# Kernel tuning notes

Measured on AMD Instinct MI355X. Metric: run time of the kernel, lower is better.

## Reference

```python
import jax, jax.numpy as jnp
import numpy as np

N = 100000        # nodes
E = 3200000       # edges (avg degree 32)
IN, HID, OUT = 512, 256, 64
K = 10
ALPHA = 0.1


def setup_inputs() -> dict:
    key = jax.random.key(0)
    k1, k2, k3, k4 = jax.random.split(key, 4)
    x = jax.random.normal(k1, (N, IN), dtype=jnp.float32)
    edge_index = jax.random.randint(k2, (2, E), 0, N, dtype=jnp.int64)
    W1 = jax.random.normal(k3, (IN, HID), dtype=jnp.float32) * (1.0 / np.sqrt(IN))
    b1 = jnp.zeros((HID,), dtype=jnp.float32)
    W2 = jax.random.normal(k4, (HID, OUT), dtype=jnp.float32) * (1.0 / np.sqrt(HID))
    b2 = jnp.zeros((OUT,), dtype=jnp.float32)
    return {"x": x, "edge_index": edge_index, "W1": W1, "b1": b1, "W2": W2, "b2": b2}


def reference(x, edge_index, W1, b1, W2, b2):
    # MLP head: Linear -> ReLU -> Linear
    h = jax.nn.relu(x @ W1 + b1)
    h = h @ W2 + b2                                   # [N, OUT]

    # gcn_norm with self-loops: D^-1/2 (A + I) D^-1/2
    src = jnp.concatenate([edge_index[0], jnp.arange(N, dtype=edge_index.dtype)])
    dst = jnp.concatenate([edge_index[1], jnp.arange(N, dtype=edge_index.dtype)])
    deg = jax.ops.segment_sum(jnp.ones_like(src, dtype=h.dtype), dst, num_segments=N)
    dinv = jnp.where(deg > 0, jax.lax.rsqrt(deg), 0.0)
    norm = dinv[src] * dinv[dst]                      # [E+N]

    h0 = h

    def step(h, _):
        msg = h[src] * norm[:, None]                  # gather + edge scale
        agg = jax.ops.segment_sum(msg, dst, num_segments=N)  # scatter-add
        h = (1.0 - ALPHA) * agg + ALPHA * h0          # teleport
        return h, None

    h, _ = jax.lax.scan(step, h, None, length=K)
    return h
```

## Files before the change

### kernel.cpp

```cpp
#include <hip/hip_runtime.h>
#include <hip/hip_bf16.h>
#include <hip/hip_fp16.h>


typedef __bf16 bf16x8 __attribute__((ext_vector_type(8)));
typedef float f32x4 __attribute__((ext_vector_type(4)));

static constexpr int IN = 512, HID = 256, OUT = 64;
static constexpr int LDT = 40;

static __device__ __forceinline__ ushort f2bf(float f) {
  __hip_bfloat16 b = __float2bfloat16(f);
  return *reinterpret_cast<ushort*>(&b);
}
static __device__ __forceinline__ float bf2f(ushort u) {
  unsigned int x = ((unsigned int)u) << 16;
  return __uint_as_float(x);
}
static __device__ __forceinline__ float h15f(unsigned int u) {
  ushort hb = (ushort)(u & 0x7FFFu);
  __half h = *reinterpret_cast<__half*>(&hb);
  return __half2float(h);
}

__global__ void transpose_f32_bf16(const float* __restrict__ in, ushort* __restrict__ out,
                                   int K, int C) {
  int idx = blockIdx.x * 256 + threadIdx.x;
  if (idx < K * C) {
    int n = idx / K, k = idx % K;
    out[idx] = f2bf(in[k * C + n]);
  }
}

__global__ __launch_bounds__(256) void gemm1(const float* __restrict__ X,
                                             const ushort* __restrict__ W1T,
                                             const float* __restrict__ b1,
                                             ushort* __restrict__ h1, int M) {
  __shared__ __align__(16) ushort As[128 * LDT];
  __shared__ __align__(16) ushort Bs[128 * LDT];
  const int tid = threadIdx.x;
  const int m0 = blockIdx.x * 128;
  const int n0 = blockIdx.y * 128;
  const int lane = tid & 63, w = tid >> 6;
  const int wr = w >> 1, wc = w & 1;
  const int lm = lane & 15, lq = lane >> 4;
  const int cB = tid & 3, rB = tid >> 2;
  const int cA = tid & 7, rA = tid >> 3;

  f32x4 acc[4][4] = {};

  for (int k0 = 0; k0 < IN; k0 += 32) {
#pragma unroll
    for (int rr = 0; rr < 4; ++rr) {
      int m = rA + rr * 32;
      int gm = m0 + m; gm = gm < M ? gm : M - 1;
      float4 f = *reinterpret_cast<const float4*>(&X[(size_t)gm * IN + k0 + cA * 4]);
      ushort4 cv;
      cv.x = f2bf(f.x); cv.y = f2bf(f.y); cv.z = f2bf(f.z); cv.w = f2bf(f.w);
      *reinterpret_cast<ushort4*>(&As[m * LDT + cA * 4]) = cv;
    }
#pragma unroll
    for (int rr = 0; rr < 2; ++rr) {
      int n = rB + rr * 64;
      *reinterpret_cast<int4*>(&Bs[n * LDT + cB * 8]) =
          *reinterpret_cast<const int4*>(&W1T[(size_t)(n0 + n) * IN + k0 + cB * 8]);
    }
    __syncthreads();
    bf16x8 af[4], bq[4];
#pragma unroll
    for (int mi = 0; mi < 4; ++mi)
      af[mi] = *reinterpret_cast<const bf16x8*>(&As[(wr * 64 + mi * 16 + lm) * LDT + lq * 8]);
#pragma unroll
    for (int ni = 0; ni < 4; ++ni)
      bq[ni] = *reinterpret_cast<const bf16x8*>(&Bs[(wc * 64 + ni * 16 + lm) * LDT + lq * 8]);
#pragma unroll
    for (int mi = 0; mi < 4; ++mi)
#pragma unroll
      for (int ni = 0; ni < 4; ++ni)
        acc[mi][ni] = __builtin_amdgcn_mfma_f32_16x16x32_bf16(af[mi], bq[ni], acc[mi][ni], 0, 0, 0);
    __syncthreads();
  }

#pragma unroll
  for (int ni = 0; ni < 4; ++ni) {
    int col = n0 + wc * 64 + ni * 16 + lm;
    float bias = b1[col];
#pragma unroll
    for (int mi = 0; mi < 4; ++mi) {
#pragma unroll
      for (int rg = 0; rg < 4; ++rg) {
        int row = m0 + wr * 64 + mi * 16 + lq * 4 + rg;
        if (row < M) {
          float v = acc[mi][ni][rg] + bias;
          v = v > 0.f ? v : 0.f;
          h1[(size_t)row * HID + col] = f2bf(v);
        }
      }
    }
  }
}

__global__ __launch_bounds__(256) void gemm2(const ushort* __restrict__ h1,
                                             const ushort* __restrict__ W2T,
                                             const float* __restrict__ b2,
                                             float* __restrict__ H0f,
                                             ushort* __restrict__ H0b, int M) {
  __shared__ __align__(16) ushort As[128 * LDT];
  __shared__ __align__(16) ushort Bs[64 * LDT];
  const int tid = threadIdx.x;
  const int m0 = blockIdx.x * 128;
  const int lane = tid & 63, w = tid >> 6;
  const int lm = lane & 15, lq = lane >> 4;
  const int c = tid & 3, r = tid >> 2;

  f32x4 acc[2][4] = {};

  for (int k0 = 0; k0 < HID; k0 += 32) {
#pragma unroll
    for (int rr = 0; rr < 2; ++rr) {
      int m = r + rr * 64;
      int gm = m0 + m; gm = gm < M ? gm : M - 1;
      *reinterpret_cast<int4*>(&As[m * LDT + c * 8]) =
          *reinterpret_cast<const int4*>(&h1[(size_t)gm * HID + k0 + c * 8]);
    }
    *reinterpret_cast<int4*>(&Bs[r * LDT + c * 8]) =
        *reinterpret_cast<const int4*>(&W2T[(size_t)r * HID + k0 + c * 8]);
    __syncthreads();
    bf16x8 af[2], bq[4];
#pragma unroll
    for (int mi = 0; mi < 2; ++mi)
      af[mi] = *reinterpret_cast<const bf16x8*>(&As[(w * 32 + mi * 16 + lm) * LDT + lq * 8]);
#pragma unroll
    for (int ni = 0; ni < 4; ++ni)
      bq[ni] = *reinterpret_cast<const bf16x8*>(&Bs[(ni * 16 + lm) * LDT + lq * 8]);
#pragma unroll
    for (int mi = 0; mi < 2; ++mi)
#pragma unroll
      for (int ni = 0; ni < 4; ++ni)
        acc[mi][ni] = __builtin_amdgcn_mfma_f32_16x16x32_bf16(af[mi], bq[ni], acc[mi][ni], 0, 0, 0);
    __syncthreads();
  }

#pragma unroll
  for (int ni = 0; ni < 4; ++ni) {
    int col = ni * 16 + lm;
    float bias = b2[col];
#pragma unroll
    for (int mi = 0; mi < 2; ++mi) {
#pragma unroll
      for (int rg = 0; rg < 4; ++rg) {
        int row = m0 + w * 32 + mi * 16 + lq * 4 + rg;
        if (row < M) {
          float v = acc[mi][ni][rg] + bias;
          H0f[(size_t)row * OUT + col] = v;
          H0b[(size_t)row * OUT + col] = f2bf(v);
        }
      }
    }
  }
}

__global__ void count_deg(const int* __restrict__ ei, int* __restrict__ cnt, int E) {
  int e = blockIdx.x * 256 + threadIdx.x;
  if (e < E) atomicAdd(&cnt[ei[E + e]], 1);
}

__global__ void calc_dinv(const int* __restrict__ cnt, float* __restrict__ dinv, int n) {
  int v = blockIdx.x * 256 + threadIdx.x;
  if (v < n) dinv[v] = rsqrtf((float)cnt[v] + 1.0f);
}

__global__ __launch_bounds__(1024) void scan_kernel(const int* __restrict__ cnt,
                                                    int* __restrict__ offs,
                                                    int* __restrict__ cursor, int n) {
  __shared__ int wsum[16];
  __shared__ int woff[16];
  __shared__ int carry_s;
  const int tid = threadIdx.x;
  const int lane = tid & 63, wid = tid >> 6;
  if (tid == 0) carry_s = 0;
  __syncthreads();
  for (int base = 0; base < n; base += 4096) {
    int i0 = base + tid * 4;
    int x[4];
#pragma unroll
    for (int j = 0; j < 4; ++j) x[j] = (i0 + j < n) ? cnt[i0 + j] : 0;
    int tsum = x[0] + x[1] + x[2] + x[3];
    int val = tsum;
#pragma unroll
    for (int d = 1; d < 64; d <<= 1) {
      int t = __shfl_up(val, d, 64);
      if (lane >= d) val += t;
    }
    if (lane == 63) wsum[wid] = val;
    __syncthreads();
    if (wid == 0) {
      int s = (lane < 16) ? wsum[lane] : 0;
      int sv = s;
#pragma unroll
      for (int d = 1; d < 16; d <<= 1) {
        int t = __shfl_up(sv, d, 64);
        if (lane >= d) sv += t;
      }
      if (lane < 16) woff[lane] = sv - s;
    }
    __syncthreads();
    int excl = carry_s + woff[wid] + (val - tsum);
#pragma unroll
    for (int j = 0; j < 4; ++j) {
      if (i0 + j < n) { offs[i0 + j] = excl; cursor[i0 + j] = excl; }
      excl += x[j];
    }
    __syncthreads();
    if (tid == 1023) carry_s = excl;
    __syncthreads();
  }
  if (tid == 0) offs[n] = carry_s;
}

__global__ void fill_csr(const int* __restrict__ ei, int* __restrict__ cursor,
                         const float* __restrict__ dinv, unsigned int* __restrict__ csr,
                         int E) {
  int e = blockIdx.x * 256 + threadIdx.x;
  if (e < E) {
    int s = ei[e], d = ei[E + e];
    int p = atomicAdd(&cursor[d], 1);
    float w = dinv[s] * dinv[d];
    __half hw = __float2half(w);
    unsigned int hb = *reinterpret_cast<ushort*>(&hw);
    csr[p] = (((unsigned int)s) << 15) | hb;
  }
}

template <bool WRITE_BF>
__global__ __launch_bounds__(256) void prop_step(const float* __restrict__ hinf,
                                                 const ushort* __restrict__ hinb,
                                                 float* __restrict__ houtf,
                                                 ushort* __restrict__ houtb,
                                                 const float* __restrict__ h0,
                                                 const int* __restrict__ offs,
                                                 const unsigned int* __restrict__ csr,
                                                 const float* __restrict__ dinv, int n) {
  int gw = (blockIdx.x * 256 + threadIdx.x) >> 6;
  int lane = threadIdx.x & 63;
  if (gw >= n) return;
  float dv = dinv[gw];
  float a[8];
  a[0] = hinf[(size_t)gw * OUT + lane] * dv * dv;
#pragma unroll
  for (int k = 1; k < 8; ++k) a[k] = 0.f;
  int e0 = offs[gw], e1 = offs[gw + 1];
  for (int base = e0; base < e1; base += 64) {
    int rem = e1 - base;
    unsigned int my = (lane < rem) ? csr[base + lane] : 0u;
    int cnt = rem < 64 ? rem : 64;
    int cnt16 = (cnt + 15) & ~15;
    for (int j = 0; j < cnt16; j += 16) {
      unsigned int u[16];
#pragma unroll
      for (int k = 0; k < 16; ++k) u[k] = (unsigned int)__shfl((int)my, j + k);
      float v[16];
#pragma unroll
      for (int k = 0; k < 16; ++k)
        v[k] = bf2f(hinb[(size_t)(u[k] >> 15) * OUT + lane]);
#pragma unroll
      for (int k = 0; k < 16; ++k) a[k & 7] = fmaf(h15f(u[k]), v[k], a[k & 7]);
    }
  }
  float acc = ((a[0] + a[1]) + (a[2] + a[3])) + ((a[4] + a[5]) + (a[6] + a[7]));
  float o = 0.9f * acc + 0.1f * h0[(size_t)gw * OUT + lane];
  houtf[(size_t)gw * OUT + lane] = o;
  if (WRITE_BF) houtb[(size_t)gw * OUT + lane] = f2bf(o);
}

extern "C" void kernel_launch(void* const* d_in, const int* in_sizes, int n_in,
                              void* d_out, int out_size, void* d_ws, size_t ws_size,
                              hipStream_t stream) {
  const float* X  = (const float*)d_in[0];
  const int*   EI = (const int*)d_in[1];
  const float* W1 = (const float*)d_in[2];
  const float* b1 = (const float*)d_in[3];
  const float* W2 = (const float*)d_in[4];
  const float* b2 = (const float*)d_in[5];
  float* out = (float*)d_out;

  const int N = in_sizes[0] / IN;
  const int E = in_sizes[1] / 2;

  char* ws = (char*)d_ws;
  size_t o = 0;
  auto alloc = [&](size_t b) {
    char* p = ws + o;
    o = (o + b + 255) & ~(size_t)255;
    return p;
  };
  float*  H0f  = (float*)alloc((size_t)N * OUT * 4);
  ushort* H0b  = (ushort*)alloc((size_t)N * OUT * 2);
  float*  hAf  = (float*)alloc((size_t)N * OUT * 4);
  ushort* hAb  = (ushort*)alloc((size_t)N * OUT * 2);
  float*  hBf  = (float*)alloc((size_t)N * OUT * 4);
  ushort* hBb  = (ushort*)alloc((size_t)N * OUT * 2);
  ushort* h1   = (ushort*)alloc((size_t)N * HID * 2);
  ushort* W1T  = (ushort*)alloc((size_t)IN * HID * 2);
  ushort* W2T  = (ushort*)alloc((size_t)HID * OUT * 2);
  int*    cnt  = (int*)alloc((size_t)N * 4);
  int*    offs = (int*)alloc((size_t)(N + 1) * 4);
  int*    curs = (int*)alloc((size_t)N * 4);
  float*  dinv = (float*)alloc((size_t)N * 4);
  unsigned int* csr = (unsigned int*)alloc((size_t)E * 4);
  (void)ws_size; (void)n_in; (void)out_size;

  transpose_f32_bf16<<<(IN * HID + 255) / 256, 256, 0, stream>>>(W1, W1T, IN, HID);
  transpose_f32_bf16<<<(HID * OUT + 255) / 256, 256, 0, stream>>>(W2, W2T, HID, OUT);

  gemm1<<<dim3((N + 127) / 128, HID / 128), 256, 0, stream>>>(X, W1T, b1, h1, N);
  gemm2<<<(N + 127) / 128, 256, 0, stream>>>(h1, W2T, b2, H0f, H0b, N);

  hipMemsetAsync(cnt, 0, (size_t)N * 4, stream);
  count_deg<<<(E + 255) / 256, 256, 0, stream>>>(EI, cnt, E);
  calc_dinv<<<(N + 255) / 256, 256, 0, stream>>>(cnt, dinv, N);
  scan_kernel<<<1, 1024, 0, stream>>>(cnt, offs, curs, N);
  fill_csr<<<(E + 255) / 256, 256, 0, stream>>>(EI, curs, dinv, csr, E);

  const int pgrid = (N * OUT + 255) / 256;
  prop_step<true><<<pgrid, 256, 0, stream>>>(H0f, H0b, hAf, hAb, H0f, offs, csr, dinv, N);
  for (int i = 0; i < 4; ++i) {
    prop_step<true><<<pgrid, 256, 0, stream>>>(hAf, hAb, hBf, hBb, H0f, offs, csr, dinv, N);
    prop_step<true><<<pgrid, 256, 0, stream>>>(hBf, hBb, hAf, hAb, H0f, offs, csr, dinv, N);
  }
  prop_step<false><<<pgrid, 256, 0, stream>>>(hAf, hAb, out, nullptr, H0f, offs, csr, dinv, N);
}
```

Measured before the change: 1.378 ms.

## Build CSR via two-phase bucketed fill with shared-memory cursors

Replaces the single-pass CSR fill, which did a global atomic per edge on per-node cursors with scattered 4-byte writes, with a two-phase scheme. Edges are first binned into 128-node buckets using per-bucket global atomics into a staging buffer, then each block places its bucket's edges into final CSR slots using shared-memory atomics. The staging buffer reuses the h1 GEMM intermediate, so the GEMMs are moved after CSR construction. This adds an extra pass over 8-byte staged records and heavy contention on bucket counters in exchange for more local writes.

```diff
diff --git a/kernel.cpp b/kernel.cpp
--- a/kernel.cpp
+++ b/kernel.cpp
@@ -8,6 +8,7 @@
 
 static constexpr int IN = 512, HID = 256, OUT = 64;
 static constexpr int LDT = 40;
+static constexpr int BSH = 7;
 
 static __device__ __forceinline__ ushort f2bf(float f) {
   __hip_bfloat16 b = __float2bfloat16(f);
@@ -218,17 +219,47 @@
   if (tid == 0) offs[n] = carry_s;
 }
 
-__global__ void fill_csr(const int* __restrict__ ei, int* __restrict__ cursor,
-                         const float* __restrict__ dinv, unsigned int* __restrict__ csr,
-                         int E) {
+__global__ void init_bcur(const int* __restrict__ offs, int* __restrict__ bcur, int nb) {
+  int b = blockIdx.x * 256 + threadIdx.x;
+  if (b < nb) bcur[b] = offs[b << BSH];
+}
+
+__global__ void fill_stage(const int* __restrict__ ei, int* __restrict__ bcur,
+                           const float* __restrict__ dinv, uint2* __restrict__ stage,
+                           int E) {
   int e = blockIdx.x * 256 + threadIdx.x;
   if (e < E) {
     int s = ei[e], d = ei[E + e];
-    int p = atomicAdd(&cursor[d], 1);
     float w = dinv[s] * dinv[d];
     __half hw = __float2half(w);
     unsigned int hb = *reinterpret_cast<ushort*>(&hw);
-    csr[p] = (((unsigned int)s) << 15) | hb;
+    int p = atomicAdd(&bcur[d >> BSH], 1);
+    uint2 rec;
+    rec.x = (((unsigned int)s) << 15) | hb;
+    rec.y = (unsigned int)d;
+    stage[p] = rec;
+  }
+}
+
+__global__ __launch_bounds__(256) void fill_csr_phase2(const uint2* __restrict__ stage,
+                                                       const int* __restrict__ offs,
+                                                       unsigned int* __restrict__ csr,
+                                                       int n) {
+  __shared__ int lcur[1 << BSH];
+  const int b = blockIdx.x;
+  const int nb0 = b << BSH;
+  int nb1 = nb0 + (1 << BSH); if (nb1 > n) nb1 = n;
+  const int t = threadIdx.x;
+  if (t < (1 << BSH)) {
+    int node = nb0 + t;
+    lcur[t] = (node < n) ? offs[node] : 0;
+  }
+  __syncthreads();
+  const int ebase = offs[nb0], eend = offs[nb1];
+  for (int i = ebase + t; i < eend; i += 256) {
+    uint2 en = stage[i];
+    int p = atomicAdd(&lcur[en.y - (unsigned int)nb0], 1);
+    csr[p] = en.x;
   }
 }
 
@@ -286,6 +317,7 @@
 
   const int N = in_sizes[0] / IN;
   const int E = in_sizes[1] / 2;
+  const int NB = (N + (1 << BSH) - 1) >> BSH;
 
   char* ws = (char*)d_ws;
   size_t o = 0;
@@ -308,19 +340,23 @@
   int*    curs = (int*)alloc((size_t)N * 4);
   float*  dinv = (float*)alloc((size_t)N * 4);
   unsigned int* csr = (unsigned int*)alloc((size_t)E * 4);
+  int*    bcur = (int*)alloc((size_t)NB * 4);
+  uint2*  stage = (uint2*)h1;
   (void)ws_size; (void)n_in; (void)out_size;
 
   transpose_f32_bf16<<<(IN * HID + 255) / 256, 256, 0, stream>>>(W1, W1T, IN, HID);
   transpose_f32_bf16<<<(HID * OUT + 255) / 256, 256, 0, stream>>>(W2, W2T, HID, OUT);
-
-  gemm1<<<dim3((N + 127) / 128, HID / 128), 256, 0, stream>>>(X, W1T, b1, h1, N);
-  gemm2<<<(N + 127) / 128, 256, 0, stream>>>(h1, W2T, b2, H0f, H0b, N);
 
   hipMemsetAsync(cnt, 0, (size_t)N * 4, stream);
   count_deg<<<(E + 255) / 256, 256, 0, stream>>>(EI, cnt, E);
   calc_dinv<<<(N + 255) / 256, 256, 0, stream>>>(cnt, dinv, N);
   scan_kernel<<<1, 1024, 0, stream>>>(cnt, offs, curs, N);
-  fill_csr<<<(E + 255) / 256, 256, 0, stream>>>(EI, curs, dinv, csr, E);
+  init_bcur<<<(NB + 255) / 256, 256, 0, stream>>>(offs, bcur, NB);
+  fill_stage<<<(E + 255) / 256, 256, 0, stream>>>(EI, bcur, dinv, stage, E);
+  fill_csr_phase2<<<NB, 256, 0, stream>>>(stage, offs, csr, N);
+
+  gemm1<<<dim3((N + 127) / 128, HID / 128), 256, 0, stream>>>(X, W1T, b1, h1, N);
+  gemm2<<<(N + 127) / 128, 256, 0, stream>>>(h1, W2T, b2, H0f, H0b, N);
 
   const int pgrid = (N * OUT + 255) / 256;
   prop_step<true><<<pgrid, 256, 0, stream>>>(H0f, H0b, hAf, hAb, H0f, offs, csr, dinv, N);
```

New measurement: 2.011 ms. +46.0%, slower.

## Split wavefront into two half-waves gathering packed bf16 pairs per edge

Applied to the files above, without the earlier changes.

The propagation kernel now has each half of the 64-lane wavefront handle alternate edges. Each lane loads a 32-bit word holding two bf16 features instead of one 16-bit value, and the two halves are combined with a cross-half shuffle. This doubles the bytes per gather load and halves the number of load instructions per edge, which targets the per-lane gather throughput. In exchange it adds a reduction shuffle at the end and splits the fp32 and bf16 output writes between the halves. Padding rounds up to 32 edges, so low-degree nodes may do more wasted lanes.

```diff
diff --git a/kernel.cpp b/kernel.cpp
--- a/kernel.cpp
+++ b/kernel.cpp
@@ -244,33 +244,53 @@
   int gw = (blockIdx.x * 256 + threadIdx.x) >> 6;
   int lane = threadIdx.x & 63;
   if (gw >= n) return;
-  float dv = dinv[gw];
-  float a[8];
-  a[0] = hinf[(size_t)gw * OUT + lane] * dv * dv;
-#pragma unroll
-  for (int k = 1; k < 8; ++k) a[k] = 0.f;
+  const unsigned int* hin32 = (const unsigned int*)hinb;
+  const int c = lane & 31;
+  const int half = lane >> 5;
+  float alo[8], ahi[8];
+#pragma unroll
+  for (int k = 0; k < 8; ++k) { alo[k] = 0.f; ahi[k] = 0.f; }
   int e0 = offs[gw], e1 = offs[gw + 1];
   for (int base = e0; base < e1; base += 64) {
     int rem = e1 - base;
     unsigned int my = (lane < rem) ? csr[base + lane] : 0u;
     int cnt = rem < 64 ? rem : 64;
-    int cnt16 = (cnt + 15) & ~15;
-    for (int j = 0; j < cnt16; j += 16) {
+    int cnt32 = (cnt + 31) & ~31;
+    for (int j = 0; j < cnt32; j += 32) {
       unsigned int u[16];
 #pragma unroll
-      for (int k = 0; k < 16; ++k) u[k] = (unsigned int)__shfl((int)my, j + k);
-      float v[16];
-#pragma unroll
       for (int k = 0; k < 16; ++k)
-        v[k] = bf2f(hinb[(size_t)(u[k] >> 15) * OUT + lane]);
-#pragma unroll
-      for (int k = 0; k < 16; ++k) a[k & 7] = fmaf(h15f(u[k]), v[k], a[k & 7]);
-    }
-  }
-  float acc = ((a[0] + a[1]) + (a[2] + a[3])) + ((a[4] + a[5]) + (a[6] + a[7]));
-  float o = 0.9f * acc + 0.1f * h0[(size_t)gw * OUT + lane];
-  houtf[(size_t)gw * OUT + lane] = o;
-  if (WRITE_BF) houtb[(size_t)gw * OUT + lane] = f2bf(o);
+        u[k] = (unsigned int)__shfl((int)my, j + 2 * k + half);
+      unsigned int v[16];
+#pragma unroll
+      for (int k = 0; k < 16; ++k)
+        v[k] = hin32[(size_t)(u[k] >> 15) * 32 + c];
+#pragma unroll
+      for (int k = 0; k < 16; ++k) {
+        float w = h15f(u[k]);
+        float f0 = __uint_as_float(v[k] << 16);
+        float f1 = __uint_as_float(v[k] & 0xFFFF0000u);
+        alo[k & 7] = fmaf(w, f0, alo[k & 7]);
+        ahi[k & 7] = fmaf(w, f1, ahi[k & 7]);
+      }
+    }
+  }
+  float a0 = ((alo[0] + alo[1]) + (alo[2] + alo[3])) + ((alo[4] + alo[5]) + (alo[6] + alo[7]));
+  float a1 = ((ahi[0] + ahi[1]) + (ahi[2] + ahi[3])) + ((ahi[4] + ahi[5]) + (ahi[6] + ahi[7]));
+  a0 += __shfl_xor(a0, 32, 64);
+  a1 += __shfl_xor(a1, 32, 64);
+  float dv = dinv[gw];
+  float2 hf = ((const float2*)hinf)[(size_t)gw * 32 + c];
+  float2 h0f = ((const float2*)h0)[(size_t)gw * 32 + c];
+  float o0 = 0.9f * (a0 + dv * dv * hf.x) + 0.1f * h0f.x;
+  float o1 = 0.9f * (a1 + dv * dv * hf.y) + 0.1f * h0f.y;
+  if (half == 0) {
+    float2 ov; ov.x = o0; ov.y = o1;
+    ((float2*)houtf)[(size_t)gw * 32 + c] = ov;
+  } else if (WRITE_BF) {
+    unsigned int pk = (unsigned int)f2bf(o0) | ((unsigned int)f2bf(o1) << 16);
+    ((unsigned int*)houtb)[(size_t)gw * 32 + c] = pk;
+  }
 }
 
 extern "C" void kernel_launch(void* const* d_in, const int* in_sizes, int n_in,
```

After: 1.368 ms. No clear change (-0.7%).
